# Kernel tuning notes

Hardware: AMD Instinct MI355X
Metric: run time of the kernel (lower is better)

Reference implementation:

```python
import jax, jax.numpy as jnp
import numpy as np

N_EMBD = 4096
N_HEAD = 2
HEAD_DIM = N_EMBD // N_HEAD  # 2048; note seq_len T must equal HEAD_DIM for the bias broadcast
B, T = 8, HEAD_DIM


def setup_inputs() -> dict:
    key = jax.random.key(0)
    ks = jax.random.split(key, 6)
    s = 1.0 / np.sqrt(N_EMBD)
    return {
        "x": jax.random.normal(ks[0], (B, T, N_EMBD), dtype=jnp.float32),
        "Wq": jax.random.normal(ks[1], (N_EMBD, N_EMBD), dtype=jnp.float32) * s,
        "Wk": jax.random.normal(ks[2], (N_EMBD, N_EMBD), dtype=jnp.float32) * s,
        "Wv": jax.random.normal(ks[3], (N_EMBD, N_EMBD), dtype=jnp.float32) * s,
        "Wo": jax.random.normal(ks[4], (N_EMBD, N_EMBD), dtype=jnp.float32) * s,
        "position_bias": jax.random.normal(ks[5], (N_HEAD, HEAD_DIM), dtype=jnp.float32) * 0.02,
    }


def reference(x, Wq, Wk, Wv, Wo, position_bias):
    Bb, Tt, C = x.shape
    H, D = N_HEAD, C // N_HEAD
    # nn.Linear(bias=False): y = x @ W.T
    q = (x @ Wq.T).reshape(Bb, Tt, H, D).transpose(0, 2, 1, 3)  # (B,H,T,D)
    k = (x @ Wk.T).reshape(Bb, Tt, H, D).transpose(0, 2, 1, 3)
    v = (x @ Wv.T).reshape(Bb, Tt, H, D).transpose(0, 2, 1, 3)
    scale = 1.0 / jnp.sqrt(jnp.asarray(D, dtype=x.dtype))
    scores = jnp.einsum("bhtd,bhsd->bhts", q, k) * scale  # (B,H,T,T)
    # position_bias (H,D) -> (1,H,1,D); broadcasts over key axis since D == T
    scores = scores + position_bias[None, :, None, :]
    atten = jax.nn.softmax(scores, axis=-1)  # mask=None, dropout=0.0 -> identity
    y = jnp.einsum("bhts,bhsd->bhtd", atten, v)  # (B,H,T,D)
    y = y.transpose(0, 2, 1, 3).reshape(Bb, Tt, C)
    y = y @ Wo.T
    return (y, atten)
```

## Files before the change

### kernel.cpp

```cpp
#include <hip/hip_runtime.h>
#include <hip/hip_bf16.h>
#include <cstdint>
#include <cstddef>


typedef short short8_t __attribute__((ext_vector_type(8)));
typedef float f32x4   __attribute__((ext_vector_type(4)));

__device__ __forceinline__ short f2bf(float f) {
  unsigned u = __builtin_bit_cast(unsigned, f);
  u = (u + 0x7FFFu + ((u >> 16) & 1u)) >> 16;
  return (short)u;
}

__device__ __forceinline__ short8_t cvt8(f32x4 a, f32x4 b) {
  short8_t r;
  r[0] = f2bf(a[0]); r[1] = f2bf(a[1]); r[2] = f2bf(a[2]); r[3] = f2bf(a[3]);
  r[4] = f2bf(b[0]); r[5] = f2bf(b[1]); r[6] = f2bf(b[2]); r[7] = f2bf(b[3]);
  return r;
}

__device__ __forceinline__ void gld_lds16(const void* g, void* l) {
  __builtin_amdgcn_global_load_lds(
      (const __attribute__((address_space(1))) void*)g,
      (__attribute__((address_space(3))) void*)l, 16, 0, 0);
}

__global__ __launch_bounds__(256)
void cvt_f32_bf16(const float* __restrict__ src, short* __restrict__ dst, int n8) {
  for (int i = blockIdx.x * blockDim.x + threadIdx.x; i < n8;
       i += gridDim.x * blockDim.x) {
    const f32x4* p = (const f32x4*)(src + (size_t)i * 8);
    f32x4 a = __builtin_nontemporal_load(p);
    f32x4 b = __builtin_nontemporal_load(p + 1);
    *(short8_t*)(dst + (size_t)i * 8) = cvt8(a, b);
  }
}

template<int MODE>
__global__ __launch_bounds__(256, 1)
void gemm256(const short* __restrict__ Ag, const short* __restrict__ Bg,
             void* __restrict__ Cg, const float* __restrict__ bias) {
  constexpr int K  = (MODE == 3 || MODE == 4) ? 2048 : 4096;
  constexpr int NS = K / 32;

  __shared__ short lds[65536];

  const int tid = threadIdx.x;

  const int bid = blockIdx.x;
  const int id  = (bid & 7) * (gridDim.x >> 3) + (bid >> 3);

  int m0, n0, z = 0;
  size_t aoff = 0, boff = 0;
  if constexpr (MODE == 3 || MODE == 4) {
    z  = id >> 6;
    m0 = ((id >> 3) & 7) << 8;
    n0 = (id & 7) << 8;
    aoff = boff = (size_t)z << 22;
  } else {
    m0 = (id >> 4) << 8;
    n0 = (id & 15) << 8;
  }

  const int l = tid & 63;
  const int w = tid >> 6;

  const int srow = l & 15;
  const int skol = (l >> 4) * 8;
  const short* ApS = Ag + aoff + (size_t)(m0 + 64 * w + srow) * K + skol;
  const short* BpS = Bg + boff + (size_t)(n0 + 64 * w + srow) * K + skol;
  short* laS = &lds[(4 * w) * 512 + l * 8];
  short* lbS = &lds[8192 + (4 * w) * 512 + l * 8];

  auto STAGE = [&](int t) {
    const int s = (t & 3) << 14;
    const size_t k = (size_t)t * 32;
#pragma unroll
    for (int j = 0; j < 4; ++j) {
      gld_lds16(ApS + (size_t)j * 16 * K + k, laS + j * 512 + s);
      gld_lds16(BpS + (size_t)j * 16 * K + k, lbS + j * 512 + s);
    }
  };

  const int aU = (w >> 1) * 8;
  const int bU = (w & 1) * 8;
  const int l8 = l * 8;

  f32x4 acc[8][8] = {};

  STAGE(0); STAGE(1); STAGE(2);

  for (int p = 0; p < NS; ++p) {
    if (p + 2 < NS)      asm volatile("s_waitcnt vmcnt(16)" ::: "memory");
    else if (p + 1 < NS) asm volatile("s_waitcnt vmcnt(8)" ::: "memory");
    else                 asm volatile("s_waitcnt vmcnt(0)" ::: "memory");
    __builtin_amdgcn_s_barrier();

    if (p + 3 < NS) STAGE(p + 3);

    const int slot = (p & 3) << 14;
    short8_t A[8], B[8];
#pragma unroll
    for (int i = 0; i < 8; ++i)
      A[i] = *(const short8_t*)&lds[slot + (aU + i) * 512 + l8];
#pragma unroll
    for (int j = 0; j < 8; ++j)
      B[j] = *(const short8_t*)&lds[slot + 8192 + (bU + j) * 512 + l8];

    __builtin_amdgcn_s_setprio(1);
#pragma unroll
    for (int m = 0; m < 8; ++m)
#pragma unroll
      for (int n = 0; n < 8; ++n)
        acc[m][n] = __builtin_amdgcn_mfma_f32_16x16x32_bf16(A[m], B[n], acc[m][n], 0, 0, 0);
    __builtin_amdgcn_s_setprio(0);
  }

  const int fr = l & 15;
  const int kq = l >> 4;
  const int wm = (w >> 1) << 7;
  const int wn = (w & 1) << 7;
#pragma unroll
  for (int m = 0; m < 8; ++m) {
#pragma unroll
    for (int n = 0; n < 8; ++n) {
#pragma unroll
      for (int r = 0; r < 4; ++r) {
        const int gm = m0 + wm + m * 16 + kq * 4 + r;
        const int gn = n0 + wn + n * 16 + fr;
        const float v = acc[m][n][r];
        if constexpr (MODE == 0) {
          short* dst = (short*)Cg;
          const int bh = ((gm >> 11) << 1) + (gn >> 11);
          __builtin_nontemporal_store(f2bf(v),
            &dst[((size_t)bh << 22) + ((size_t)(gm & 2047) << 11) + (gn & 2047)]);
        } else if constexpr (MODE == 2) {
          short* dst = (short*)Cg;
          const int bh = ((gm >> 11) << 1) + (gn >> 11);
          __builtin_nontemporal_store(f2bf(v),
            &dst[((size_t)bh << 22) + ((size_t)(gn & 2047) << 11) + (gm & 2047)]);
        } else if constexpr (MODE == 3) {
          float* dst = (float*)Cg;
          const float sv = v * 0.022097086912079608f + bias[((z & 1) << 11) + gn];
          __builtin_nontemporal_store(sv,
            &dst[((size_t)z << 22) + ((size_t)gm << 11) + gn]);
        } else if constexpr (MODE == 4) {
          short* dst = (short*)Cg;
          const size_t row = ((size_t)(z >> 1) << 11) + gm;
          __builtin_nontemporal_store(f2bf(v),
            &dst[(row << 12) + ((size_t)(z & 1) << 11) + gn]);
        } else {
          float* dst = (float*)Cg;
          __builtin_nontemporal_store(v, &dst[(size_t)gm * 4096 + gn]);
        }
      }
    }
  }
}

__global__ __launch_bounds__(256)
void softmax_rows(float* __restrict__ attn, short* __restrict__ outb) {
  float* row  = attn + ((size_t)blockIdx.x << 11);
  short* rowb = outb + ((size_t)blockIdx.x << 11);
  const int tid = threadIdx.x;

  f32x4 v0 = __builtin_nontemporal_load((const f32x4*)(row + tid * 8));
  f32x4 v1 = __builtin_nontemporal_load((const f32x4*)(row + tid * 8 + 4));

  float m = fmaxf(fmaxf(fmaxf(v0[0], v0[1]), fmaxf(v0[2], v0[3])),
                  fmaxf(fmaxf(v1[0], v1[1]), fmaxf(v1[2], v1[3])));
#pragma unroll
  for (int off = 1; off < 64; off <<= 1) m = fmaxf(m, __shfl_xor(m, off));

  __shared__ float redm[4];
  __shared__ float reds[4];
  if ((tid & 63) == 0) redm[tid >> 6] = m;
  __syncthreads();
  m = fmaxf(fmaxf(redm[0], redm[1]), fmaxf(redm[2], redm[3]));

  float e[8];
#pragma unroll
  for (int i = 0; i < 4; ++i) e[i]     = expf(v0[i] - m);
#pragma unroll
  for (int i = 0; i < 4; ++i) e[4 + i] = expf(v1[i] - m);
  float s = 0.f;
#pragma unroll
  for (int i = 0; i < 8; ++i) s += e[i];
#pragma unroll
  for (int off = 1; off < 64; off <<= 1) s += __shfl_xor(s, off);
  if ((tid & 63) == 0) reds[tid >> 6] = s;
  __syncthreads();
  s = reds[0] + reds[1] + reds[2] + reds[3];

  const float inv = 1.0f / s;
  f32x4 o0, o1;
#pragma unroll
  for (int i = 0; i < 4; ++i) { o0[i] = e[i] * inv; o1[i] = e[4 + i] * inv; }
  __builtin_nontemporal_store(o0, (f32x4*)(row + tid * 8));
  __builtin_nontemporal_store(o1, (f32x4*)(row + tid * 8 + 4));
  *(short8_t*)(rowb + tid * 8) = cvt8(o0, o1);
}

extern "C" void kernel_launch(void* const* d_in, const int* in_sizes, int n_in,
                              void* d_out, int out_size, void* d_ws, size_t ws_size,
                              hipStream_t stream) {
  const float* x  = (const float*)d_in[0];
  const float* Wq = (const float*)d_in[1];
  const float* Wk = (const float*)d_in[2];
  const float* Wv = (const float*)d_in[3];
  const float* Wo = (const float*)d_in[4];
  const float* pb = (const float*)d_in[5];

  float* y_out = (float*)d_out;
  float* attn  = y_out + (size_t)8 * 2048 * 4096;

  const size_t NEED = 4ull * 67108864ull * 2ull;
  if (ws_size < NEED) return;
  short* buf0 = (short*)d_ws;
  short* buf1 = buf0 + 67108864;
  short* buf2 = buf1 + 67108864;
  short* buf3 = buf2 + 67108864;

  short* xb      = buf0;
  short* qb      = buf1;
  short* kb      = buf2;
  short* vtb     = buf3;
  short* wob     = buf0;
  short* attn_bf = buf1;
  short* yb      = buf2;
  short* wb      = (short*)attn;

  const dim3 blk(256);
  const dim3 gcv(2048);
  const dim3 g1k(1024);

  cvt_f32_bf16<<<gcv, blk, 0, stream>>>(x, xb, 67108864 / 8);

  cvt_f32_bf16<<<gcv, blk, 0, stream>>>(Wq, wb, 16777216 / 8);
  gemm256<0><<<g1k, blk, 0, stream>>>(xb, wb, qb, nullptr);
  cvt_f32_bf16<<<gcv, blk, 0, stream>>>(Wk, wb, 16777216 / 8);
  gemm256<0><<<g1k, blk, 0, stream>>>(xb, wb, kb, nullptr);
  cvt_f32_bf16<<<gcv, blk, 0, stream>>>(Wv, wb, 16777216 / 8);
  gemm256<2><<<g1k, blk, 0, stream>>>(xb, wb, vtb, nullptr);

  cvt_f32_bf16<<<gcv, blk, 0, stream>>>(Wo, wob, 16777216 / 8);

  gemm256<3><<<g1k, blk, 0, stream>>>(qb, kb, attn, pb);
  softmax_rows<<<dim3(32768), blk, 0, stream>>>(attn, attn_bf);
  gemm256<4><<<g1k, blk, 0, stream>>>(attn_bf, vtb, yb, nullptr);
  gemm256<5><<<g1k, blk, 0, stream>>>(yb, wob, y_out, nullptr);
}
```

Measured before the change: 3.347 ms.

## Restructure GEMM to 1024-thread blocks with 16 waves and double buffering

```diff
diff --git a/kernel.cpp b/kernel.cpp
--- a/kernel.cpp
+++ b/kernel.cpp
@@ -38,13 +38,13 @@
 }
 
 template<int MODE>
-__global__ __launch_bounds__(256, 1)
+__global__ __launch_bounds__(1024, 4)
 void gemm256(const short* __restrict__ Ag, const short* __restrict__ Bg,
              void* __restrict__ Cg, const float* __restrict__ bias) {
   constexpr int K  = (MODE == 3 || MODE == 4) ? 2048 : 4096;
   constexpr int NS = K / 32;
 
-  __shared__ short lds[65536];
+  __shared__ short lds[32768];
 
   const int tid = threadIdx.x;
 
@@ -68,91 +68,81 @@
 
   const int srow = l & 15;
   const int skol = (l >> 4) * 8;
-  const short* ApS = Ag + aoff + (size_t)(m0 + 64 * w + srow) * K + skol;
-  const short* BpS = Bg + boff + (size_t)(n0 + 64 * w + srow) * K + skol;
-  short* laS = &lds[(4 * w) * 512 + l * 8];
-  short* lbS = &lds[8192 + (4 * w) * 512 + l * 8];
+  const short* ApS = Ag + aoff + (size_t)(m0 + 16 * w + srow) * K + skol;
+  const short* BpS = Bg + boff + (size_t)(n0 + 16 * w + srow) * K + skol;
+  short* lA = &lds[w * 512 + l * 8];
+  short* lB = &lds[8192 + w * 512 + l * 8];
 
   auto STAGE = [&](int t) {
-    const int s = (t & 3) << 14;
-    const size_t k = (size_t)t * 32;
-#pragma unroll
-    for (int j = 0; j < 4; ++j) {
-      gld_lds16(ApS + (size_t)j * 16 * K + k, laS + j * 512 + s);
-      gld_lds16(BpS + (size_t)j * 16 * K + k, lbS + j * 512 + s);
-    }
+    const int s = (t & 1) << 14;
+    const int k = t * 32;
+    gld_lds16(ApS + k, lA + s);
+    gld_lds16(BpS + k, lB + s);
   };
 
-  const int aU = (w >> 1) * 8;
-  const int bU = (w & 1) * 8;
+  const int aU = (w >> 2) * 4;
+  const int bU = (w & 3) * 4;
   const int l8 = l * 8;
 
-  f32x4 acc[8][8] = {};
-
-  STAGE(0); STAGE(1); STAGE(2);
+  f32x4 acc[4][4] = {};
+
+  STAGE(0);
 
   for (int p = 0; p < NS; ++p) {
-    if (p + 2 < NS)      asm volatile("s_waitcnt vmcnt(16)" ::: "memory");
-    else if (p + 1 < NS) asm volatile("s_waitcnt vmcnt(8)" ::: "memory");
-    else                 asm volatile("s_waitcnt vmcnt(0)" ::: "memory");
+    asm volatile("s_waitcnt vmcnt(0)" ::: "memory");
     __builtin_amdgcn_s_barrier();
-
-    if (p + 3 < NS) STAGE(p + 3);
-
-    const int slot = (p & 3) << 14;
-    short8_t A[8], B[8];
-#pragma unroll
-    for (int i = 0; i < 8; ++i)
+    if (p + 1 < NS) STAGE(p + 1);
+
+    const int slot = (p & 1) << 14;
+    short8_t A[4], B[4];
+#pragma unroll
+    for (int i = 0; i < 4; ++i)
       A[i] = *(const short8_t*)&lds[slot + (aU + i) * 512 + l8];
 #pragma unroll
-    for (int j = 0; j < 8; ++j)
+    for (int j = 0; j < 4; ++j)
       B[j] = *(const short8_t*)&lds[slot + 8192 + (bU + j) * 512 + l8];
 
     __builtin_amdgcn_s_setprio(1);
 #pragma unroll
-    for (int m = 0; m < 8; ++m)
-#pragma unroll
-      for (int n = 0; n < 8; ++n)
-        acc[m][n] = __builtin_amdgcn_mfma_f32_16x16x32_bf16(A[m], B[n], acc[m][n], 0, 0, 0);
+    for (int i = 0; i < 4; ++i)
+#pragma unroll
+      for (int j = 0; j < 4; ++j)
+        acc[i][j] = __builtin_amdgcn_mfma_f32_16x16x32_bf16(A[i], B[j], acc[i][j], 0, 0, 0);
     __builtin_amdgcn_s_setprio(0);
   }
 
   const int fr = l & 15;
   const int kq = l >> 4;
-  const int wm = (w >> 1) << 7;
-  const int wn = (w & 1) << 7;
-#pragma unroll
-  for (int m = 0; m < 8; ++m) {
-#pragma unroll
-    for (int n = 0; n < 8; ++n) {
+  const int wm = (w >> 2) << 6;
+  const int wn = (w & 3) << 6;
+#pragma unroll
+  for (int i = 0; i < 4; ++i) {
+#pragma unroll
+    for (int j = 0; j < 4; ++j) {
 #pragma unroll
       for (int r = 0; r < 4; ++r) {
-        const int gm = m0 + wm + m * 16 + kq * 4 + r;
-        const int gn = n0 + wn + n * 16 + fr;
-        const float v = acc[m][n][r];
+        const int gm = m0 + wm + i * 16 + kq * 4 + r;
+        const int gn = n0 + wn + j * 16 + fr;
+        const float v = acc[i][j][r];
         if constexpr (MODE == 0) {
           short* dst = (short*)Cg;
           const int bh = ((gm >> 11) << 1) + (gn >> 11);
-          __builtin_nontemporal_store(f2bf(v),
-            &dst[((size_t)bh << 22) + ((size_t)(gm & 2047) << 11) + (gn & 2047)]);
+          dst[((size_t)bh << 22) + ((size_t)(gm & 2047) << 11) + (gn & 2047)] = f2bf(v);
         } else if constexpr (MODE == 2) {
           short* dst = (short*)Cg;
           const int bh = ((gm >> 11) << 1) + (gn >> 11);
-          __builtin_nontemporal_store(f2bf(v),
-            &dst[((size_t)bh << 22) + ((size_t)(gn & 2047) << 11) + (gm & 2047)]);
+          dst[((size_t)bh << 22) + ((size_t)(gn & 2047) << 11) + (gm & 2047)] = f2bf(v);
         } else if constexpr (MODE == 3) {
           float* dst = (float*)Cg;
           const float sv = v * 0.022097086912079608f + bias[((z & 1) << 11) + gn];
-          __builtin_nontemporal_store(sv,
-            &dst[((size_t)z << 22) + ((size_t)gm << 11) + gn]);
+          dst[((size_t)z << 22) + ((size_t)gm << 11) + gn] = sv;
         } else if constexpr (MODE == 4) {
           short* dst = (short*)Cg;
           const size_t row = ((size_t)(z >> 1) << 11) + gm;
-          __builtin_nontemporal_store(f2bf(v),
-            &dst[(row << 12) + ((size_t)(z & 1) << 11) + gn]);
+          dst[(row << 12) + ((size_t)(z & 1) << 11) + gn] = f2bf(v);
         } else {
           float* dst = (float*)Cg;
-          __builtin_nontemporal_store(v, &dst[(size_t)gm * 4096 + gn]);
+          dst[(size_t)gm * 4096 + gn] = v;
         }
       }
     }
@@ -165,8 +155,8 @@
   short* rowb = outb + ((size_t)blockIdx.x << 11);
   const int tid = threadIdx.x;
 
-  f32x4 v0 = __builtin_nontemporal_load((const f32x4*)(row + tid * 8));
-  f32x4 v1 = __builtin_nontemporal_load((const f32x4*)(row + tid * 8 + 4));
+  f32x4 v0 = *(const f32x4*)(row + tid * 8);
+  f32x4 v1 = *(const f32x4*)(row + tid * 8 + 4);
 
   float m = fmaxf(fmaxf(fmaxf(v0[0], v0[1]), fmaxf(v0[2], v0[3])),
                   fmaxf(fmaxf(v1[0], v1[1]), fmaxf(v1[2], v1[3])));
@@ -197,8 +187,8 @@
   f32x4 o0, o1;
 #pragma unroll
   for (int i = 0; i < 4; ++i) { o0[i] = e[i] * inv; o1[i] = e[4 + i] * inv; }
-  __builtin_nontemporal_store(o0, (f32x4*)(row + tid * 8));
-  __builtin_nontemporal_store(o1, (f32x4*)(row + tid * 8 + 4));
+  *(f32x4*)(row + tid * 8)     = o0;
+  *(f32x4*)(row + tid * 8 + 4) = o1;
   *(short8_t*)(rowb + tid * 8) = cvt8(o0, o1);
 }
 
@@ -231,6 +221,7 @@
   short* yb      = buf2;
   short* wb      = (short*)attn;
 
+  const dim3 blk1k(1024);
   const dim3 blk(256);
   const dim3 gcv(2048);
   const dim3 g1k(1024);
@@ -238,16 +229,16 @@
   cvt_f32_bf16<<<gcv, blk, 0, stream>>>(x, xb, 67108864 / 8);
 
   cvt_f32_bf16<<<gcv, blk, 0, stream>>>(Wq, wb, 16777216 / 8);
-  gemm256<0><<<g1k, blk, 0, stream>>>(xb, wb, qb, nullptr);
+  gemm256<0><<<g1k, blk1k, 0, stream>>>(xb, wb, qb, nullptr);
   cvt_f32_bf16<<<gcv, blk, 0, stream>>>(Wk, wb, 16777216 / 8);
-  gemm256<0><<<g1k, blk, 0, stream>>>(xb, wb, kb, nullptr);
+  gemm256<0><<<g1k, blk1k, 0, stream>>>(xb, wb, kb, nullptr);
   cvt_f32_bf16<<<gcv, blk, 0, stream>>>(Wv, wb, 16777216 / 8);
-  gemm256<2><<<g1k, blk, 0, stream>>>(xb, wb, vtb, nullptr);
+  gemm256<2><<<g1k, blk1k, 0, stream>>>(xb, wb, vtb, nullptr);
 
   cvt_f32_bf16<<<gcv, blk, 0, stream>>>(Wo, wob, 16777216 / 8);
 
-  gemm256<3><<<g1k, blk, 0, stream>>>(qb, kb, attn, pb);
+  gemm256<3><<<g1k, blk1k, 0, stream>>>(qb, kb, attn, pb);
   softmax_rows<<<dim3(32768), blk, 0, stream>>>(attn, attn_bf);
-  gemm256<4><<<g1k, blk, 0, stream>>>(attn_bf, vtb, yb, nullptr);
-  gemm256<5><<<g1k, blk, 0, stream>>>(yb, wob, y_out, nullptr);
-}
+  gemm256<4><<<g1k, blk1k, 0, stream>>>(attn_bf, vtb, yb, nullptr);
+  gemm256<5><<<g1k, blk1k, 0, stream>>>(yb, wob, y_out, nullptr);
+}
```

Result: slower. 3.548 ms (+6.0%).
